# Performance work log

Hardware: AMD Instinct MI355X
Metric: run time of the kernel (lower is better)

Reference implementation:

```python
import jax, jax.numpy as jnp
import numpy as np
import math

L, H, C, T_MAX, VP = 12, 12, 768, 1024, 50304
D = C // H  # head dim = 64
EPS = 1e-5


def layer_norm(x, w, b):
    mu = jnp.mean(x, axis=-1, keepdims=True)
    var = jnp.mean(jnp.square(x - mu), axis=-1, keepdims=True)
    return (x - mu) * jax.lax.rsqrt(var + EPS) * w + b


def setup_inputs() -> dict:
    key = jax.random.key(0)
    ks = jax.random.split(key, 20)
    s = 0.02
    B, T = 2, 1024
    inp = {
        'idx': jax.random.randint(ks[0], (B, T), 0, VP),
        'wte': jax.random.normal(ks[1], (VP, C), jnp.float32) * s,
        'wpe': jax.random.normal(ks[2], (T_MAX, C), jnp.float32) * s,
        'ln1w': jnp.ones((L, C), jnp.float32),
        'ln1b': jnp.zeros((L, C), jnp.float32),
        'qkvw': jax.random.normal(ks[3], (L, 3 * C, C), jnp.float32) * s,
        'qkvb': jnp.zeros((L, 3 * C), jnp.float32),
        'projw': jax.random.normal(ks[4], (L, C, C), jnp.float32) * s,
        'projb': jnp.zeros((L, C), jnp.float32),
        'ln2w': jnp.ones((L, C), jnp.float32),
        'ln2b': jnp.zeros((L, C), jnp.float32),
        'fcw': jax.random.normal(ks[5], (L, 4 * C, C), jnp.float32) * s,
        'fcb': jnp.zeros((L, 4 * C), jnp.float32),
        'fcprojw': jax.random.normal(ks[6], (L, C, 4 * C), jnp.float32) * s,
        'fcprojb': jnp.zeros((L, C), jnp.float32),
        'lnfw': jnp.ones((C,), jnp.float32),
        'lnfb': jnp.zeros((C,), jnp.float32),
    }
    return inp


def _block(x, p, mask):
    ln1w, ln1b, qkvw, qkvb, projw, projb, ln2w, ln2b, fcw, fcb, fcprojw, fcprojb = p
    B, T, _ = x.shape
    # --- causal self-attention (naive O(T^2)) ---
    h = layer_norm(x, ln1w, ln1b)
    qkv = h @ qkvw.T + qkvb                      # (B,T,3C)
    q, k, v = jnp.split(qkv, 3, axis=-1)
    q = q.reshape(B, T, H, D).transpose(0, 2, 1, 3)  # (B,H,T,D)
    k = k.reshape(B, T, H, D).transpose(0, 2, 1, 3)
    v = v.reshape(B, T, H, D).transpose(0, 2, 1, 3)
    att = jnp.einsum('bhqd,bhkd->bhqk', q, k) * (1.0 / math.sqrt(D))
    att = jnp.where(mask, att, jnp.float32(-jnp.inf))
    att = jax.nn.softmax(att, axis=-1)
    y = jnp.einsum('bhqk,bhkd->bhqd', att, v)
    y = y.transpose(0, 2, 1, 3).reshape(B, T, C)
    x = x + y @ projw.T + projb
    # --- MLP ---
    h2 = layer_norm(x, ln2w, ln2b)
    h2 = jax.nn.gelu(h2 @ fcw.T + fcb, approximate=True)
    x = x + h2 @ fcprojw.T + fcprojb
    return x


def reference(idx, wte, wpe, ln1w, ln1b, qkvw, qkvb, projw, projb,
              ln2w, ln2b, fcw, fcb, fcprojw, fcprojb, lnfw, lnfb):
    B, T = idx.shape
    x = wte[idx] + wpe[:T]                      # (B,T,C)
    mask = jnp.tril(jnp.ones((T, T), bool))[None, None]
    params = (ln1w, ln1b, qkvw, qkvb, projw, projb,
              ln2w, ln2b, fcw, fcb, fcprojw, fcprojb)

    def step(x, p):
        return _block(x, p, mask), None

    x, _ = jax.lax.scan(step, x, params)
    x = layer_norm(x, lnfw, lnfb)
    logits = x @ wte.T                           # tied lm_head, (B,T,Vp)
    return logits
```

## Files before the change

### kernel.cpp

```cpp
#include <hip/hip_runtime.h>
#include <hip/hip_bf16.h>
#include <math.h>

#define BB 2
#define TT 1024
#define CC 768
#define NH 12
#define HD 64
#define NL 12
#define VP 50304
#define MM (BB * TT)

typedef _Float16 half8 __attribute__((ext_vector_type(8)));
typedef float floatx4 __attribute__((ext_vector_type(4)));

__device__ __forceinline__ float gelu_tanh(float x) {
    const float k = 0.7978845608028654f;
    float x3 = x * x * x;
    return 0.5f * x * (1.0f + tanhf(k * (x + 0.044715f * x3)));
}

__device__ __forceinline__ half8 cvt8(float4 a, float4 b) {
    half8 h;
    h[0] = (_Float16)a.x; h[1] = (_Float16)a.y;
    h[2] = (_Float16)a.z; h[3] = (_Float16)a.w;
    h[4] = (_Float16)b.x; h[5] = (_Float16)b.y;
    h[6] = (_Float16)b.z; h[7] = (_Float16)b.w;
    return h;
}

__global__ void embed_kernel(const int* __restrict__ idx,
                             const float* __restrict__ wte,
                             const float* __restrict__ wpe,
                             float* __restrict__ x, int n) {
    int i = blockIdx.x * blockDim.x + threadIdx.x;
    if (i >= n) return;
    int c = i % CC;
    int bt = i / CC;
    int t = bt % TT;
    x[i] = wte[(size_t)idx[bt] * CC + c] + wpe[(size_t)t * CC + c];
}

__launch_bounds__(256)
__global__ void ln_kernel(const float* __restrict__ x,
                          const float* __restrict__ w,
                          const float* __restrict__ b,
                          float* __restrict__ out) {
    int row = blockIdx.x;
    int tid = threadIdx.x;
    const float* xr = x + (size_t)row * CC;
    __shared__ float red[256];
    float v0 = xr[tid], v1 = xr[tid + 256], v2 = xr[tid + 512];
    red[tid] = v0 + v1 + v2;
    __syncthreads();
    for (int s = 128; s > 0; s >>= 1) {
        if (tid < s) red[tid] += red[tid + s];
        __syncthreads();
    }
    float mu = red[0] * (1.0f / CC);
    __syncthreads();
    float d0 = v0 - mu, d1 = v1 - mu, d2 = v2 - mu;
    red[tid] = d0 * d0 + d1 * d1 + d2 * d2;
    __syncthreads();
    for (int s = 128; s > 0; s >>= 1) {
        if (tid < s) red[tid] += red[tid + s];
        __syncthreads();
    }
    float rstd = rsqrtf(red[0] * (1.0f / CC) + 1e-5f);
    float* outr = out + (size_t)row * CC;
    outr[tid]       = d0 * rstd * w[tid]       + b[tid];
    outr[tid + 256] = d1 * rstd * w[tid + 256] + b[tid + 256];
    outr[tid + 512] = d2 * rstd * w[tid + 512] + b[tid + 512];
}

template <int BM, int BN, bool GELU, bool RES>
__launch_bounds__(256)
__global__ void gemm_kernel(const float* __restrict__ A,
                            const float* __restrict__ W,
                            const float* __restrict__ bias,
                            const float* __restrict__ res,
                            float* __restrict__ out,
                            int M, int N, int K) {
    __shared__ __align__(16) _Float16 As[BM * 32];
    __shared__ __align__(16) _Float16 Ws[BN * 32];
    half8* As8 = (half8*)As;
    half8* Ws8 = (half8*)Ws;

    constexpr int FI = BM / 32;
    constexpr int FJ = BN / 32;

    const int tid  = threadIdx.x;
    const int lane = tid & 63;
    const int wid  = tid >> 6;
    const int wr   = (wid >> 1) * (BM / 2);
    const int wc   = (wid & 1) * (BN / 2);
    const int g    = lane >> 4;
    const int c16  = lane & 15;

    const int nwg = gridDim.x;
    const int hw  = blockIdx.x;
    const int xcd = hw & 7;
    const int q   = nwg >> 3, r = nwg & 7;
    const int logical =
        (xcd < r ? xcd * (q + 1) : r * (q + 1) + (xcd - r) * q) + (hw >> 3);
    const int mblocks = M / BM;
    const int bm = (logical % mblocks) * BM;
    const int bn = (logical / mblocks) * BN;

    floatx4 acc[FI][FJ] = {};

    if constexpr (BM == 128) {
        const int sr  = tid >> 1;
        const int sc0 = (tid & 1) * 2;
        const int sz  = (sr >> 1) & 3;
        const float* Ap = A + (size_t)(bm + sr) * K + sc0 * 8;
        const float* Wp = W + (size_t)(bn + sr) * K + sc0 * 8;
        for (int k0 = 0; k0 < K; k0 += 32) {
            float4 a0 = *(const float4*)(Ap + k0);
            float4 a1 = *(const float4*)(Ap + k0 + 4);
            float4 a2 = *(const float4*)(Ap + k0 + 8);
            float4 a3 = *(const float4*)(Ap + k0 + 12);
            float4 w0 = *(const float4*)(Wp + k0);
            float4 w1 = *(const float4*)(Wp + k0 + 4);
            float4 w2 = *(const float4*)(Wp + k0 + 8);
            float4 w3 = *(const float4*)(Wp + k0 + 12);
            __syncthreads();
            As8[sr * 4 + (sc0 ^ sz)]       = cvt8(a0, a1);
            As8[sr * 4 + ((sc0 + 1) ^ sz)] = cvt8(a2, a3);
            Ws8[sr * 4 + (sc0 ^ sz)]       = cvt8(w0, w1);
            Ws8[sr * 4 + ((sc0 + 1) ^ sz)] = cvt8(w2, w3);
            __syncthreads();
            half8 af[FI], bf[FJ];
#pragma unroll
            for (int i = 0; i < FI; ++i) {
                int ra = wr + i * 16 + c16;
                af[i] = As8[ra * 4 + (g ^ ((ra >> 1) & 3))];
            }
#pragma unroll
            for (int j = 0; j < FJ; ++j) {
                int rb = wc + j * 16 + c16;
                bf[j] = Ws8[rb * 4 + (g ^ ((rb >> 1) & 3))];
            }
#pragma unroll
            for (int i = 0; i < FI; ++i)
#pragma unroll
                for (int j = 0; j < FJ; ++j)
                    acc[i][j] = __builtin_amdgcn_mfma_f32_16x16x32_f16(
                        af[i], bf[j], acc[i][j], 0, 0, 0);
        }
    } else {
        const int sr = tid >> 2;
        const int sc = tid & 3;
        const int sz = (sr >> 1) & 3;
        const float* Ap = A + (size_t)(bm + sr) * K + sc * 8;
        const float* Wp = W + (size_t)(bn + sr) * K + sc * 8;
        for (int k0 = 0; k0 < K; k0 += 32) {
            float4 a0 = *(const float4*)(Ap + k0);
            float4 a1 = *(const float4*)(Ap + k0 + 4);
            float4 w0 = *(const float4*)(Wp + k0);
            float4 w1 = *(const float4*)(Wp + k0 + 4);
            __syncthreads();
            As8[sr * 4 + (sc ^ sz)] = cvt8(a0, a1);
            Ws8[sr * 4 + (sc ^ sz)] = cvt8(w0, w1);
            __syncthreads();
            half8 af[FI], bf[FJ];
#pragma unroll
            for (int i = 0; i < FI; ++i) {
                int ra = wr + i * 16 + c16;
                af[i] = As8[ra * 4 + (g ^ ((ra >> 1) & 3))];
            }
#pragma unroll
            for (int j = 0; j < FJ; ++j) {
                int rb = wc + j * 16 + c16;
                bf[j] = Ws8[rb * 4 + (g ^ ((rb >> 1) & 3))];
            }
#pragma unroll
            for (int i = 0; i < FI; ++i)
#pragma unroll
                for (int j = 0; j < FJ; ++j)
                    acc[i][j] = __builtin_amdgcn_mfma_f32_16x16x32_f16(
                        af[i], bf[j], acc[i][j], 0, 0, 0);
        }
    }

#pragma unroll
    for (int i = 0; i < FI; ++i) {
#pragma unroll
        for (int j = 0; j < FJ; ++j) {
#pragma unroll
            for (int r = 0; r < 4; ++r) {
                int row = bm + wr + i * 16 + g * 4 + r;
                int col = bn + wc + j * 16 + c16;
                float v = acc[i][j][r];
                if (bias) v += bias[col];
                if (GELU) v = gelu_tanh(v);
                if (RES) v += res[(size_t)row * N + col];
                out[(size_t)row * N + col] = v;
            }
        }
    }
}

__launch_bounds__(256)
__global__ void attn_kernel(const float* __restrict__ qkv,
                            float* __restrict__ y) {
    __shared__ __align__(16) _Float16 Ks[64][80];
    __shared__ __align__(16) _Float16 Vt[64][80];
    __shared__ __align__(16) _Float16 Pl[4][16][80];

    const int tid  = threadIdx.x;
    const int lane = tid & 63;
    const int w    = tid >> 6;
    const int g    = lane >> 4;
    const int c    = lane & 15;

    const int qt = blockIdx.x & 15;
    const int h  = (blockIdx.x >> 4) % NH;
    const int b  = blockIdx.x / (16 * NH);

    const size_t rstride = 3 * CC;
    const float* qbase = qkv + (size_t)(b * TT) * rstride + h * HD;
    const float* kbase = qbase + CC;
    const float* vbase = qbase + 2 * CC;

    half8 qf[2];
    {
        const float* qrow = qbase + (size_t)(qt * 64 + w * 16 + c) * rstride;
#pragma unroll
        for (int ks = 0; ks < 2; ++ks) {
            float4 x0 = *(const float4*)(qrow + 32 * ks + 8 * g);
            float4 x1 = *(const float4*)(qrow + 32 * ks + 8 * g + 4);
            half8 hv;
            hv[0] = (_Float16)(x0.x * 0.125f); hv[1] = (_Float16)(x0.y * 0.125f);
            hv[2] = (_Float16)(x0.z * 0.125f); hv[3] = (_Float16)(x0.w * 0.125f);
            hv[4] = (_Float16)(x1.x * 0.125f); hv[5] = (_Float16)(x1.y * 0.125f);
            hv[6] = (_Float16)(x1.z * 0.125f); hv[7] = (_Float16)(x1.w * 0.125f);
            qf[ks] = hv;
        }
    }

    float mrow[4] = {-1e30f, -1e30f, -1e30f, -1e30f};
    float lrow[4] = {0.0f, 0.0f, 0.0f, 0.0f};
    floatx4 accO[4] = {};

    const int srow = tid >> 2;
    const int scol = (tid & 3) * 16;

    for (int kt = 0; kt <= qt; ++kt) {
        __syncthreads();
        {
            const float* kr = kbase + (size_t)(kt * 64 + srow) * rstride + scol;
            float4 k0 = *(const float4*)(kr);
            float4 k1 = *(const float4*)(kr + 4);
            float4 k2 = *(const float4*)(kr + 8);
            float4 k3 = *(const float4*)(kr + 12);
            *(half8*)&Ks[srow][scol]     = cvt8(k0, k1);
            *(half8*)&Ks[srow][scol + 8] = cvt8(k2, k3);
            const float* vr = vbase + (size_t)(kt * 64 + srow) * rstride + scol;
#pragma unroll
            for (int q4 = 0; q4 < 4; ++q4) {
                float4 v = *(const float4*)(vr + 4 * q4);
                Vt[scol + 4 * q4 + 0][srow] = (_Float16)v.x;
                Vt[scol + 4 * q4 + 1][srow] = (_Float16)v.y;
                Vt[scol + 4 * q4 + 2][srow] = (_Float16)v.z;
                Vt[scol + 4 * q4 + 3][srow] = (_Float16)v.w;
            }
        }
        __syncthreads();

        floatx4 sf[4] = {};
#pragma unroll
        for (int ks = 0; ks < 2; ++ks) {
#pragma unroll
            for (int j = 0; j < 4; ++j) {
                half8 kf = *(const half8*)&Ks[16 * j + c][32 * ks + 8 * g];
                sf[j] = __builtin_amdgcn_mfma_f32_16x16x32_f16(
                    qf[ks], kf, sf[j], 0, 0, 0);
            }
        }
        if (kt == qt) {
#pragma unroll
            for (int j = 0; j < 4; ++j)
#pragma unroll
                for (int r = 0; r < 4; ++r)
                    if (16 * j + c > w * 16 + 4 * g + r) sf[j][r] = -1e30f;
        }

        float rm[4];
#pragma unroll
        for (int r = 0; r < 4; ++r)
            rm[r] = fmaxf(fmaxf(sf[0][r], sf[1][r]), fmaxf(sf[2][r], sf[3][r]));
#pragma unroll
        for (int off = 1; off < 16; off <<= 1)
#pragma unroll
            for (int r = 0; r < 4; ++r)
                rm[r] = fmaxf(rm[r], __shfl_xor(rm[r], off));

        float corr[4];
#pragma unroll
        for (int r = 0; r < 4; ++r) {
            float mn = fmaxf(mrow[r], rm[r]);
            corr[r] = __expf(mrow[r] - mn);
            mrow[r] = mn;
        }
        float ps[4][4];
#pragma unroll
        for (int j = 0; j < 4; ++j)
#pragma unroll
            for (int r = 0; r < 4; ++r)
                ps[j][r] = __expf(sf[j][r] - mrow[r]);
        float rs[4];
#pragma unroll
        for (int r = 0; r < 4; ++r)
            rs[r] = (ps[0][r] + ps[1][r]) + (ps[2][r] + ps[3][r]);
#pragma unroll
        for (int off = 1; off < 16; off <<= 1)
#pragma unroll
            for (int r = 0; r < 4; ++r)
                rs[r] += __shfl_xor(rs[r], off);
#pragma unroll
        for (int r = 0; r < 4; ++r)
            lrow[r] = lrow[r] * corr[r] + rs[r];
#pragma unroll
        for (int jd = 0; jd < 4; ++jd)
#pragma unroll
            for (int r = 0; r < 4; ++r)
                accO[jd][r] *= corr[r];

#pragma unroll
        for (int j = 0; j < 4; ++j)
#pragma unroll
            for (int r = 0; r < 4; ++r)
                Pl[w][4 * g + r][16 * j + c] = (_Float16)ps[j][r];

#pragma unroll
        for (int ks = 0; ks < 2; ++ks) {
            half8 pa = *(const half8*)&Pl[w][c][32 * ks + 8 * g];
#pragma unroll
            for (int jd = 0; jd < 4; ++jd) {
                half8 vb = *(const half8*)&Vt[16 * jd + c][32 * ks + 8 * g];
                accO[jd] = __builtin_amdgcn_mfma_f32_16x16x32_f16(
                    pa, vb, accO[jd], 0, 0, 0);
            }
        }
    }

#pragma unroll
    for (int jd = 0; jd < 4; ++jd)
#pragma unroll
        for (int r = 0; r < 4; ++r) {
            int q = qt * 64 + w * 16 + 4 * g + r;
            y[((size_t)(b * TT + q)) * CC + h * HD + 16 * jd + c] =
                accO[jd][r] / lrow[r];
        }
}

extern "C" void kernel_launch(void* const* d_in, const int* in_sizes, int n_in,
                              void* d_out, int out_size, void* d_ws, size_t ws_size,
                              hipStream_t stream) {
    const int*   idx     = (const int*)d_in[0];
    const float* wte     = (const float*)d_in[1];
    const float* wpe     = (const float*)d_in[2];
    const float* ln1w    = (const float*)d_in[3];
    const float* ln1b    = (const float*)d_in[4];
    const float* qkvw    = (const float*)d_in[5];
    const float* qkvb    = (const float*)d_in[6];
    const float* projw   = (const float*)d_in[7];
    const float* projb   = (const float*)d_in[8];
    const float* ln2w    = (const float*)d_in[9];
    const float* ln2b    = (const float*)d_in[10];
    const float* fcw     = (const float*)d_in[11];
    const float* fcb     = (const float*)d_in[12];
    const float* fcprojw = (const float*)d_in[13];
    const float* fcprojb = (const float*)d_in[14];
    const float* lnfw    = (const float*)d_in[15];
    const float* lnfb    = (const float*)d_in[16];
    float* logits = (float*)d_out;

    float* ws = (float*)d_ws;
    const size_t xn = (size_t)MM * CC;
    float* x   = ws;
    float* h   = x + xn;
    float* y   = h + xn;
    float* big = y + xn;
    float* qkv = big;
    float* hfc = big;

    const int M = MM;
    dim3 tb(256);

    {
        int n = (int)xn;
        embed_kernel<<<(n + 255) / 256, tb, 0, stream>>>(idx, wte, wpe, x, n);
    }

    const int nb_qkv    = (M / 128) * (3 * CC / 128);
    const int nb_proj   = (M / 64) * (CC / 64);
    const int nb_fc     = (M / 128) * (4 * CC / 128);
    const int nb_fcproj = (M / 64) * (CC / 64);
    const int nb_head   = (M / 128) * (VP / 128);

    for (int l = 0; l < NL; ++l) {
        ln_kernel<<<M, tb, 0, stream>>>(x, ln1w + l * CC, ln1b + l * CC, h);
        gemm_kernel<128, 128, false, false><<<dim3(nb_qkv), tb, 0, stream>>>(
            h, qkvw + (size_t)l * 3 * CC * CC, qkvb + (size_t)l * 3 * CC,
            nullptr, qkv, M, 3 * CC, CC);
        attn_kernel<<<dim3(BB * NH * (TT / 64)), tb, 0, stream>>>(qkv, y);
        gemm_kernel<64, 64, false, true><<<dim3(nb_proj), tb, 0, stream>>>(
            y, projw + (size_t)l * CC * CC, projb + (size_t)l * CC,
            x, x, M, CC, CC);
        ln_kernel<<<M, tb, 0, stream>>>(x, ln2w + l * CC, ln2b + l * CC, h);
        gemm_kernel<128, 128, true, false><<<dim3(nb_fc), tb, 0, stream>>>(
            h, fcw + (size_t)l * 4 * CC * CC, fcb + (size_t)l * 4 * CC,
            nullptr, hfc, M, 4 * CC, CC);
        gemm_kernel<64, 64, false, true><<<dim3(nb_fcproj), tb, 0, stream>>>(
            hfc, fcprojw + (size_t)l * CC * 4 * CC, fcprojb + (size_t)l * CC,
            x, x, M, CC, 4 * CC);
    }

    ln_kernel<<<M, tb, 0, stream>>>(x, lnfw, lnfb, h);
    gemm_kernel<128, 128, false, false><<<dim3(nb_head), tb, 0, stream>>>(
        h, wte, nullptr, nullptr, logits, M, VP, CC);
}
```

Before: 4.199 ms.

## Double-buffer GEMM and attention tiles, add nontemporal logits stores, cheaper GELU

Both GEMM paths and the attention kernel now keep two LDS buffers and prefetch the next K-slice or K/V tile into registers while the current one is consumed. This removes one barrier per iteration and overlaps global loads with MFMA work, at the cost of doubled LDS use, which may lower occupancy. The lm_head GEMM writes logits with nontemporal stores to avoid polluting the cache with the large output. GELU's tanh is replaced by an exp-based formula using __expf.

New measurement: 3.872 ms. -7.8%, faster.

```diff
diff --git a/kernel.cpp b/kernel.cpp
--- a/kernel.cpp
+++ b/kernel.cpp
@@ -16,8 +16,10 @@
 
 __device__ __forceinline__ float gelu_tanh(float x) {
     const float k = 0.7978845608028654f;
-    float x3 = x * x * x;
-    return 0.5f * x * (1.0f + tanhf(k * (x + 0.044715f * x3)));
+    float u = k * x * (1.0f + 0.044715f * x * x);
+    float e = __expf(2.0f * u);
+    float t = 1.0f - 2.0f / (e + 1.0f);
+    return 0.5f * x * (1.0f + t);
 }
 
 __device__ __forceinline__ half8 cvt8(float4 a, float4 b) {
@@ -73,7 +75,7 @@
     outr[tid + 512] = d2 * rstd * w[tid + 512] + b[tid + 512];
 }
 
-template <int BM, int BN, bool GELU, bool RES>
+template <int BM, int BN, bool GELU, bool RES, bool NT>
 __launch_bounds__(256)
 __global__ void gemm_kernel(const float* __restrict__ A,
                             const float* __restrict__ W,
@@ -81,8 +83,8 @@
                             const float* __restrict__ res,
                             float* __restrict__ out,
                             int M, int N, int K) {
-    __shared__ __align__(16) _Float16 As[BM * 32];
-    __shared__ __align__(16) _Float16 Ws[BN * 32];
+    __shared__ __align__(16) _Float16 As[2 * BM * 32];
+    __shared__ __align__(16) _Float16 Ws[2 * BN * 32];
     half8* As8 = (half8*)As;
     half8* Ws8 = (half8*)Ws;
 
@@ -115,31 +117,42 @@
         const int sz  = (sr >> 1) & 3;
         const float* Ap = A + (size_t)(bm + sr) * K + sc0 * 8;
         const float* Wp = W + (size_t)(bn + sr) * K + sc0 * 8;
+        float4 a0 = *(const float4*)(Ap);
+        float4 a1 = *(const float4*)(Ap + 4);
+        float4 a2 = *(const float4*)(Ap + 8);
+        float4 a3 = *(const float4*)(Ap + 12);
+        float4 w0 = *(const float4*)(Wp);
+        float4 w1 = *(const float4*)(Wp + 4);
+        float4 w2 = *(const float4*)(Wp + 8);
+        float4 w3 = *(const float4*)(Wp + 12);
         for (int k0 = 0; k0 < K; k0 += 32) {
-            float4 a0 = *(const float4*)(Ap + k0);
-            float4 a1 = *(const float4*)(Ap + k0 + 4);
-            float4 a2 = *(const float4*)(Ap + k0 + 8);
-            float4 a3 = *(const float4*)(Ap + k0 + 12);
-            float4 w0 = *(const float4*)(Wp + k0);
-            float4 w1 = *(const float4*)(Wp + k0 + 4);
-            float4 w2 = *(const float4*)(Wp + k0 + 8);
-            float4 w3 = *(const float4*)(Wp + k0 + 12);
+            half8* Acur = As8 + ((k0 >> 5) & 1) * (BM * 4);
+            half8* Wcur = Ws8 + ((k0 >> 5) & 1) * (BN * 4);
+            Acur[sr * 4 + (sc0 ^ sz)]       = cvt8(a0, a1);
+            Acur[sr * 4 + ((sc0 + 1) ^ sz)] = cvt8(a2, a3);
+            Wcur[sr * 4 + (sc0 ^ sz)]       = cvt8(w0, w1);
+            Wcur[sr * 4 + ((sc0 + 1) ^ sz)] = cvt8(w2, w3);
             __syncthreads();
-            As8[sr * 4 + (sc0 ^ sz)]       = cvt8(a0, a1);
-            As8[sr * 4 + ((sc0 + 1) ^ sz)] = cvt8(a2, a3);
-            Ws8[sr * 4 + (sc0 ^ sz)]       = cvt8(w0, w1);
-            Ws8[sr * 4 + ((sc0 + 1) ^ sz)] = cvt8(w2, w3);
-            __syncthreads();
+            if (k0 + 32 < K) {
+                a0 = *(const float4*)(Ap + k0 + 32);
+                a1 = *(const float4*)(Ap + k0 + 36);
+                a2 = *(const float4*)(Ap + k0 + 40);
+                a3 = *(const float4*)(Ap + k0 + 44);
+                w0 = *(const float4*)(Wp + k0 + 32);
+                w1 = *(const float4*)(Wp + k0 + 36);
+                w2 = *(const float4*)(Wp + k0 + 40);
+                w3 = *(const float4*)(Wp + k0 + 44);
+            }
             half8 af[FI], bf[FJ];
 #pragma unroll
             for (int i = 0; i < FI; ++i) {
                 int ra = wr + i * 16 + c16;
-                af[i] = As8[ra * 4 + (g ^ ((ra >> 1) & 3))];
+                af[i] = Acur[ra * 4 + (g ^ ((ra >> 1) & 3))];
             }
 #pragma unroll
             for (int j = 0; j < FJ; ++j) {
                 int rb = wc + j * 16 + c16;
-                bf[j] = Ws8[rb * 4 + (g ^ ((rb >> 1) & 3))];
+                bf[j] = Wcur[rb * 4 + (g ^ ((rb >> 1) & 3))];
             }
 #pragma unroll
             for (int i = 0; i < FI; ++i)
@@ -154,25 +167,32 @@
         const int sz = (sr >> 1) & 3;
         const float* Ap = A + (size_t)(bm + sr) * K + sc * 8;
         const float* Wp = W + (size_t)(bn + sr) * K + sc * 8;
+        float4 a0 = *(const float4*)(Ap);
+        float4 a1 = *(const float4*)(Ap + 4);
+        float4 w0 = *(const float4*)(Wp);
+        float4 w1 = *(const float4*)(Wp + 4);
         for (int k0 = 0; k0 < K; k0 += 32) {
-            float4 a0 = *(const float4*)(Ap + k0);
-            float4 a1 = *(const float4*)(Ap + k0 + 4);
-            float4 w0 = *(const float4*)(Wp + k0);
-            float4 w1 = *(const float4*)(Wp + k0 + 4);
+            half8* Acur = As8 + ((k0 >> 5) & 1) * (BM * 4);
+            half8* Wcur = Ws8 + ((k0 >> 5) & 1) * (BN * 4);
+            Acur[sr * 4 + (sc ^ sz)] = cvt8(a0, a1);
+            Wcur[sr * 4 + (sc ^ sz)] = cvt8(w0, w1);
             __syncthreads();
-            As8[sr * 4 + (sc ^ sz)] = cvt8(a0, a1);
-            Ws8[sr * 4 + (sc ^ sz)] = cvt8(w0, w1);
-            __syncthreads();
+            if (k0 + 32 < K) {
+                a0 = *(const float4*)(Ap + k0 + 32);
+                a1 = *(const float4*)(Ap + k0 + 36);
+                w0 = *(const float4*)(Wp + k0 + 32);
+                w1 = *(const float4*)(Wp + k0 + 36);
+            }
             half8 af[FI], bf[FJ];
 #pragma unroll
             for (int i = 0; i < FI; ++i) {
                 int ra = wr + i * 16 + c16;
-                af[i] = As8[ra * 4 + (g ^ ((ra >> 1) & 3))];
+                af[i] = Acur[ra * 4 + (g ^ ((ra >> 1) & 3))];
             }
 #pragma unroll
             for (int j = 0; j < FJ; ++j) {
                 int rb = wc + j * 16 + c16;
-                bf[j] = Ws8[rb * 4 + (g ^ ((rb >> 1) & 3))];
+                bf[j] = Wcur[rb * 4 + (g ^ ((rb >> 1) & 3))];
             }
 #pragma unroll
             for (int i = 0; i < FI; ++i)
@@ -195,7 +215,10 @@
                 if (bias) v += bias[col];
                 if (GELU) v = gelu_tanh(v);
                 if (RES) v += res[(size_t)row * N + col];
-                out[(size_t)row * N + col] = v;
+                if (NT)
+                    __builtin_nontemporal_store(v, &out[(size_t)row * N + col]);
+                else
+                    out[(size_t)row * N + col] = v;
             }
         }
     }
@@ -204,8 +227,8 @@
 __launch_bounds__(256)
 __global__ void attn_kernel(const float* __restrict__ qkv,
                             float* __restrict__ y) {
-    __shared__ __align__(16) _Float16 Ks[64][80];
-    __shared__ __align__(16) _Float16 Vt[64][80];
+    __shared__ __align__(16) _Float16 Ks[2][64][80];
+    __shared__ __align__(16) _Float16 Vt[2][64][80];
     __shared__ __align__(16) _Float16 Pl[4][16][80];
 
     const int tid  = threadIdx.x;
@@ -246,34 +269,60 @@
     const int srow = tid >> 2;
     const int scol = (tid & 3) * 16;
 
+    float4 kA, kB, kC, kD, vA, vB, vC, vD;
+    {
+        const float* kr = kbase + (size_t)srow * rstride + scol;
+        kA = *(const float4*)(kr);
+        kB = *(const float4*)(kr + 4);
+        kC = *(const float4*)(kr + 8);
+        kD = *(const float4*)(kr + 12);
+        const float* vr = vbase + (size_t)srow * rstride + scol;
+        vA = *(const float4*)(vr);
+        vB = *(const float4*)(vr + 4);
+        vC = *(const float4*)(vr + 8);
+        vD = *(const float4*)(vr + 12);
+    }
+
     for (int kt = 0; kt <= qt; ++kt) {
+        const int cur = kt & 1;
+        *(half8*)&Ks[cur][srow][scol]     = cvt8(kA, kB);
+        *(half8*)&Ks[cur][srow][scol + 8] = cvt8(kC, kD);
+        Vt[cur][scol +  0][srow] = (_Float16)vA.x;
+        Vt[cur][scol +  1][srow] = (_Float16)vA.y;
+        Vt[cur][scol +  2][srow] = (_Float16)vA.z;
+        Vt[cur][scol +  3][srow] = (_Float16)vA.w;
+        Vt[cur][scol +  4][srow] = (_Float16)vB.x;
+        Vt[cur][scol +  5][srow] = (_Float16)vB.y;
+        Vt[cur][scol +  6][srow] = (_Float16)vB.z;
+        Vt[cur][scol +  7][srow] = (_Float16)vB.w;
+        Vt[cur][scol +  8][srow] = (_Float16)vC.x;
+        Vt[cur][scol +  9][srow] = (_Float16)vC.y;
+        Vt[cur][scol + 10][srow] = (_Float16)vC.z;
+        Vt[cur][scol + 11][srow] = (_Float16)vC.w;
+        Vt[cur][scol + 12][srow] = (_Float16)vD.x;
+        Vt[cur][scol + 13][srow] = (_Float16)vD.y;
+        Vt[cur][scol + 14][srow] = (_Float16)vD.z;
+        Vt[cur][scol + 15][srow] = (_Float16)vD.w;
         __syncthreads();
-        {
-            const float* kr = kbase + (size_t)(kt * 64 + srow) * rstride + scol;
-            float4 k0 = *(const float4*)(kr);
-            float4 k1 = *(const float4*)(kr + 4);
-            float4 k2 = *(const float4*)(kr + 8);
-            float4 k3 = *(const float4*)(kr + 12);
-            *(half8*)&Ks[srow][scol]     = cvt8(k0, k1);
-            *(half8*)&Ks[srow][scol + 8] = cvt8(k2, k3);
-            const float* vr = vbase + (size_t)(kt * 64 + srow) * rstride + scol;
-#pragma unroll
-            for (int q4 = 0; q4 < 4; ++q4) {
-                float4 v = *(const float4*)(vr + 4 * q4);
-                Vt[scol + 4 * q4 + 0][srow] = (_Float16)v.x;
-                Vt[scol + 4 * q4 + 1][srow] = (_Float16)v.y;
-                Vt[scol + 4 * q4 + 2][srow] = (_Float16)v.z;
-                Vt[scol + 4 * q4 + 3][srow] = (_Float16)v.w;
-            }
-        }
-        __syncthreads();
+        if (kt < qt) {
+            const float* kr = kbase + (size_t)((kt + 1) * 64 + srow) * rstride + scol;
+            kA = *(const float4*)(kr);
+            kB = *(const float4*)(kr + 4);
+            kC = *(const float4*)(kr + 8);
+            kD = *(const float4*)(kr + 12);
+            const float* vr = vbase + (size_t)((kt + 1) * 64 + srow) * rstride + scol;
+            vA = *(const float4*)(vr);
+            vB = *(const float4*)(vr + 4);
+            vC = *(const float4*)(vr + 8);
+            vD = *(const float4*)(vr + 12);
+        }
 
         floatx4 sf[4] = {};
 #pragma unroll
         for (int ks = 0; ks < 2; ++ks) {
 #pragma unroll
             for (int j = 0; j < 4; ++j) {
-                half8 kf = *(const half8*)&Ks[16 * j + c][32 * ks + 8 * g];
+                half8 kf = *(const half8*)&Ks[cur][16 * j + c][32 * ks + 8 * g];
                 sf[j] = __builtin_amdgcn_mfma_f32_16x16x32_f16(
                     qf[ks], kf, sf[j], 0, 0, 0);
             }
@@ -338,7 +387,7 @@
             half8 pa = *(const half8*)&Pl[w][c][32 * ks + 8 * g];
 #pragma unroll
             for (int jd = 0; jd < 4; ++jd) {
-                half8 vb = *(const half8*)&Vt[16 * jd + c][32 * ks + 8 * g];
+                half8 vb = *(const half8*)&Vt[cur][16 * jd + c][32 * ks + 8 * g];
                 accO[jd] = __builtin_amdgcn_mfma_f32_16x16x32_f16(
                     pa, vb, accO[jd], 0, 0, 0);
             }
@@ -402,23 +451,23 @@
 
     for (int l = 0; l < NL; ++l) {
         ln_kernel<<<M, tb, 0, stream>>>(x, ln1w + l * CC, ln1b + l * CC, h);
-        gemm_kernel<128, 128, false, false><<<dim3(nb_qkv), tb, 0, stream>>>(
+        gemm_kernel<128, 128, false, false, false><<<dim3(nb_qkv), tb, 0, stream>>>(
             h, qkvw + (size_t)l * 3 * CC * CC, qkvb + (size_t)l * 3 * CC,
             nullptr, qkv, M, 3 * CC, CC);
         attn_kernel<<<dim3(BB * NH * (TT / 64)), tb, 0, stream>>>(qkv, y);
-        gemm_kernel<64, 64, false, true><<<dim3(nb_proj), tb, 0, stream>>>(
+        gemm_kernel<64, 64, false, true, false><<<dim3(nb_proj), tb, 0, stream>>>(
             y, projw + (size_t)l * CC * CC, projb + (size_t)l * CC,
             x, x, M, CC, CC);
         ln_kernel<<<M, tb, 0, stream>>>(x, ln2w + l * CC, ln2b + l * CC, h);
-        gemm_kernel<128, 128, true, false><<<dim3(nb_fc), tb, 0, stream>>>(
+        gemm_kernel<128, 128, true, false, false><<<dim3(nb_fc), tb, 0, stream>>>(
             h, fcw + (size_t)l * 4 * CC * CC, fcb + (size_t)l * 4 * CC,
             nullptr, hfc, M, 4 * CC, CC);
-        gemm_kernel<64, 64, false, true><<<dim3(nb_fcproj), tb, 0, stream>>>(
+        gemm_kernel<64, 64, false, true, false><<<dim3(nb_fcproj), tb, 0, stream>>>(
             hfc, fcprojw + (size_t)l * CC * 4 * CC, fcprojb + (size_t)l * CC,
             x, x, M, CC, 4 * CC);
     }
 
     ln_kernel<<<M, tb, 0, stream>>>(x, lnfw, lnfb, h);
-    gemm_kernel<128, 128, false, false><<<dim3(nb_head), tb, 0, stream>>>(
+    gemm_kernel<128, 128, false, false, true><<<dim3(nb_head), tb, 0, stream>>>(
         h, wte, nullptr, nullptr, logits, M, VP, CC);
 }
```
